# Performance work log

Hardware: AMD Instinct MI355X
Metric: run time of the kernel (lower is better)

The kernel has to match this reference:

```python
import jax, jax.numpy as jnp
import numpy as np

B, NF, EC, H, W = 16, 64, 3, 256, 256
NF1, NF2 = NF // 8, NF // 4  # 8, 16

def _leaky(x):
    return jnp.where(x >= 0, x, 0.2 * x)

def setup_inputs() -> dict:
    key = jax.random.key(0)
    ks = jax.random.split(key, 10)
    s = lambda fan_in: 1.0 / np.sqrt(fan_in)
    return {
        "feature_maps": jax.random.normal(ks[0], (B, NF, H, W), dtype=jnp.float32),
        "extra_maps": jax.random.normal(ks[1], (B, EC, H, W), dtype=jnp.float32),
        "w1": jax.random.uniform(ks[2], (NF1, EC), jnp.float32, -s(EC), s(EC)),
        "b1": jax.random.uniform(ks[3], (NF1,), jnp.float32, -s(EC), s(EC)),
        "w2": jax.random.uniform(ks[4], (NF2, NF1), jnp.float32, -s(NF1), s(NF1)),
        "b2": jax.random.uniform(ks[5], (NF2,), jnp.float32, -s(NF1), s(NF1)),
        "wm": jax.random.uniform(ks[6], (NF, NF2), jnp.float32, -s(NF2), s(NF2)),
        "bm": jax.random.uniform(ks[7], (NF,), jnp.float32, -s(NF2), s(NF2)),
        "wa": jax.random.uniform(ks[8], (NF, NF2), jnp.float32, -s(NF2), s(NF2)),
        "ba": jax.random.uniform(ks[9], (NF,), jnp.float32, -s(NF2), s(NF2)),
    }

def reference(feature_maps, extra_maps, w1, b1, w2, b2, wm, bm, wa, ba):
    # 1x1 convs expressed as channel contractions (per-pixel MLP chain)
    fea1 = _leaky(jnp.einsum('oc,bchw->bohw', w1, extra_maps) + b1[:, None, None])
    fea2 = _leaky(jnp.einsum('oc,bchw->bohw', w2, fea1) + b2[:, None, None])
    mul = jnp.einsum('oc,bchw->bohw', wm, fea2) + bm[:, None, None]
    add = jnp.einsum('oc,bchw->bohw', wa, fea2) + ba[:, None, None]
    # out = add / (1 + feature_maps * mul)
    return add / (1.0 + feature_maps * mul)
```

## Files before the change

kernel.cpp:

```cpp
#include <hip/hip_runtime.h>

#define HW 65536
#define NPIX (16 * HW)
#define THREADS 256


__device__ __forceinline__ double leakyd(double x) {
    return fmax(x, 0.2 * x);
}

__global__ __launch_bounds__(THREADS, 4) void attcnn_kernel(
    const float* __restrict__ fm,
    const float* __restrict__ ex,
    const float* __restrict__ w1,
    const float* __restrict__ b1,
    const float* __restrict__ w2,
    const float* __restrict__ b2,
    const float* __restrict__ wm,
    const float* __restrict__ bm,
    const float* __restrict__ wa,
    const float* __restrict__ ba,
    float* __restrict__ out)
{
    __shared__ double s_w1[24];
    __shared__ double s_b1[8];
    __shared__ double s_w2[128];
    __shared__ double s_b2[16];
    __shared__ double s_wm[1024];
    __shared__ double s_bm[64];
    __shared__ float  s_wa[1024];
    __shared__ float  s_ba[64];

    const int tid = threadIdx.x;
    if (tid < 24)  s_w1[tid] = (double)w1[tid];
    if (tid < 8)   s_b1[tid] = (double)b1[tid];
    if (tid < 128) s_w2[tid] = (double)w2[tid];
    if (tid < 16)  s_b2[tid] = (double)b2[tid];
    if (tid < 64)  { s_bm[tid] = (double)bm[tid]; s_ba[tid] = ba[tid]; }
    #pragma unroll
    for (int i = 0; i < 4; ++i) {
        s_wm[tid + i * 256] = (double)wm[tid + i * 256];
        s_wa[tid + i * 256] = wa[tid + i * 256];
    }
    __syncthreads();

    const int idx = blockIdx.x * THREADS + tid;
    const int b   = idx >> 16;
    const int hw  = idx & 65535;

    const float* exp_ = ex + (long)b * 3 * HW + hw;
    const double e0 = (double)exp_[0];
    const double e1 = (double)exp_[HW];
    const double e2 = (double)exp_[2 * HW];

    double f1v[8];
    #pragma unroll
    for (int j = 0; j < 8; ++j) {
        f1v[j] = leakyd(fma(s_w1[j * 3 + 0], e0,
                        fma(s_w1[j * 3 + 1], e1,
                        fma(s_w1[j * 3 + 2], e2, s_b1[j]))));
    }

    double f2d[16];
    float  f2s[16];
    #pragma unroll
    for (int k = 0; k < 16; ++k) {
        double acc = s_b2[k];
        #pragma unroll
        for (int j = 0; j < 8; ++j)
            acc = fma(s_w2[k * 8 + j], f1v[j], acc);
        acc = leakyd(acc);
        f2d[k] = acc;
        f2s[k] = (float)acc;
    }

    const float* fmp = fm  + (long)b * 64 * HW + hw;
    float*       op  = out + (long)b * 64 * HW + hw;

    float fcur[8], fnxt[8];
    #pragma unroll
    for (int i = 0; i < 8; ++i) fcur[i] = fmp[(long)i * HW];

    #pragma unroll 1
    for (int c = 0; c < 8; ++c) {
        const int ob = c * 8;
        if (c < 7) {
            #pragma unroll
            for (int i = 0; i < 8; ++i)
                fnxt[i] = fmp[(long)(ob + 8 + i) * HW];
        }
        #pragma unroll
        for (int i = 0; i < 8; ++i) {
            const int o = ob + i;
            double m = s_bm[o];
            float  a = s_ba[o];
            #pragma unroll
            for (int k = 0; k < 16; ++k) {
                m = fma(s_wm[o * 16 + k], f2d[k], m);
                a = fmaf(s_wa[o * 16 + k], f2s[k], a);
            }
            const double den = fma((double)fcur[i], m, 1.0);
            float h = (float)den;
            float r = __builtin_amdgcn_rcpf(h);
            r = r * fmaf(-h, r, 2.0f);
            op[(long)o * HW] = a * r;
        }
        if (c < 7) {
            #pragma unroll
            for (int i = 0; i < 8; ++i) fcur[i] = fnxt[i];
        }
    }
}

extern "C" void kernel_launch(void* const* d_in, const int* in_sizes, int n_in,
                              void* d_out, int out_size, void* d_ws, size_t ws_size,
                              hipStream_t stream) {
    const float* fm = (const float*)d_in[0];
    const float* ex = (const float*)d_in[1];
    const float* w1 = (const float*)d_in[2];
    const float* b1 = (const float*)d_in[3];
    const float* w2 = (const float*)d_in[4];
    const float* b2 = (const float*)d_in[5];
    const float* wm = (const float*)d_in[6];
    const float* bm = (const float*)d_in[7];
    const float* wa = (const float*)d_in[8];
    const float* ba = (const float*)d_in[9];
    float* out = (float*)d_out;

    const int blocks = NPIX / THREADS;
    attcnn_kernel<<<blocks, THREADS, 0, stream>>>(fm, ex, w1, b1, w2, b2,
                                                  wm, bm, wa, ba, out);
}
```

Before: 473.3 us.

## Pre-convert weights in a setup kernel, read them uniformly, stream loads nontemporally

Adds a small kernel that converts the weights to double and float once into workspace. The main kernel then reads them straight from global memory with uniform addresses, which the compiler can turn into scalar loads, instead of staging them through shared memory behind a per-block barrier. Feature-map loads and output stores become nontemporal to reduce cache pollution. The mul/add channel dot products are split into two accumulators to shorten FMA dependency chains. This costs one extra kernel launch and relies on scalar caching of the weights.

```diff
diff --git a/kernel.cpp b/kernel.cpp
--- a/kernel.cpp
+++ b/kernel.cpp
@@ -5,46 +5,49 @@
 #define THREADS 256
 
 
+#define DW1 0
+#define DB1 24
+#define DW2 32
+#define DB2 160
+#define DWM 176
+#define DBM 1200
+#define NDBL 1264
+#define FWA 0
+#define FBA 1024
+
 __device__ __forceinline__ double leakyd(double x) {
     return fmax(x, 0.2 * x);
+}
+
+__global__ __launch_bounds__(256) void cvt_weights(
+    const float* __restrict__ w1, const float* __restrict__ b1,
+    const float* __restrict__ w2, const float* __restrict__ b2,
+    const float* __restrict__ wm, const float* __restrict__ bm,
+    const float* __restrict__ wa, const float* __restrict__ ba,
+    double* __restrict__ wd, float* __restrict__ wf)
+{
+    const int t = threadIdx.x;
+    if (t < 24)  wd[DW1 + t] = (double)w1[t];
+    if (t < 8)   wd[DB1 + t] = (double)b1[t];
+    if (t < 128) wd[DW2 + t] = (double)w2[t];
+    if (t < 16)  wd[DB2 + t] = (double)b2[t];
+    if (t < 64)  wd[DBM + t] = (double)bm[t];
+    if (t < 64)  wf[FBA + t] = ba[t];
+    #pragma unroll
+    for (int i = 0; i < 4; ++i) {
+        wd[DWM + t + i * 256] = (double)wm[t + i * 256];
+        wf[FWA + t + i * 256] = wa[t + i * 256];
+    }
 }
 
 __global__ __launch_bounds__(THREADS, 4) void attcnn_kernel(
     const float* __restrict__ fm,
     const float* __restrict__ ex,
-    const float* __restrict__ w1,
-    const float* __restrict__ b1,
-    const float* __restrict__ w2,
-    const float* __restrict__ b2,
-    const float* __restrict__ wm,
-    const float* __restrict__ bm,
-    const float* __restrict__ wa,
-    const float* __restrict__ ba,
+    const double* __restrict__ wd,
+    const float* __restrict__ wf,
     float* __restrict__ out)
 {
-    __shared__ double s_w1[24];
-    __shared__ double s_b1[8];
-    __shared__ double s_w2[128];
-    __shared__ double s_b2[16];
-    __shared__ double s_wm[1024];
-    __shared__ double s_bm[64];
-    __shared__ float  s_wa[1024];
-    __shared__ float  s_ba[64];
-
-    const int tid = threadIdx.x;
-    if (tid < 24)  s_w1[tid] = (double)w1[tid];
-    if (tid < 8)   s_b1[tid] = (double)b1[tid];
-    if (tid < 128) s_w2[tid] = (double)w2[tid];
-    if (tid < 16)  s_b2[tid] = (double)b2[tid];
-    if (tid < 64)  { s_bm[tid] = (double)bm[tid]; s_ba[tid] = ba[tid]; }
-    #pragma unroll
-    for (int i = 0; i < 4; ++i) {
-        s_wm[tid + i * 256] = (double)wm[tid + i * 256];
-        s_wa[tid + i * 256] = wa[tid + i * 256];
-    }
-    __syncthreads();
-
-    const int idx = blockIdx.x * THREADS + tid;
+    const int idx = blockIdx.x * THREADS + threadIdx.x;
     const int b   = idx >> 16;
     const int hw  = idx & 65535;
 
@@ -56,19 +59,19 @@
     double f1v[8];
     #pragma unroll
     for (int j = 0; j < 8; ++j) {
-        f1v[j] = leakyd(fma(s_w1[j * 3 + 0], e0,
-                        fma(s_w1[j * 3 + 1], e1,
-                        fma(s_w1[j * 3 + 2], e2, s_b1[j]))));
+        f1v[j] = leakyd(fma(wd[DW1 + j * 3 + 0], e0,
+                        fma(wd[DW1 + j * 3 + 1], e1,
+                        fma(wd[DW1 + j * 3 + 2], e2, wd[DB1 + j]))));
     }
 
     double f2d[16];
     float  f2s[16];
     #pragma unroll
     for (int k = 0; k < 16; ++k) {
-        double acc = s_b2[k];
+        double acc = wd[DB2 + k];
         #pragma unroll
         for (int j = 0; j < 8; ++j)
-            acc = fma(s_w2[k * 8 + j], f1v[j], acc);
+            acc = fma(wd[DW2 + k * 8 + j], f1v[j], acc);
         acc = leakyd(acc);
         f2d[k] = acc;
         f2s[k] = (float)acc;
@@ -79,7 +82,8 @@
 
     float fcur[8], fnxt[8];
     #pragma unroll
-    for (int i = 0; i < 8; ++i) fcur[i] = fmp[(long)i * HW];
+    for (int i = 0; i < 8; ++i)
+        fcur[i] = __builtin_nontemporal_load(fmp + (long)i * HW);
 
     #pragma unroll 1
     for (int c = 0; c < 8; ++c) {
@@ -87,23 +91,29 @@
         if (c < 7) {
             #pragma unroll
             for (int i = 0; i < 8; ++i)
-                fnxt[i] = fmp[(long)(ob + 8 + i) * HW];
+                fnxt[i] = __builtin_nontemporal_load(fmp + (long)(ob + 8 + i) * HW);
         }
         #pragma unroll
         for (int i = 0; i < 8; ++i) {
             const int o = ob + i;
-            double m = s_bm[o];
-            float  a = s_ba[o];
+            const double* wmr = wd + DWM + o * 16;
+            const float*  war = wf + FWA + o * 16;
+            double m0 = wd[DBM + o], m1 = 0.0;
+            float  a0 = wf[FBA + o], a1 = 0.0f;
             #pragma unroll
-            for (int k = 0; k < 16; ++k) {
-                m = fma(s_wm[o * 16 + k], f2d[k], m);
-                a = fmaf(s_wa[o * 16 + k], f2s[k], a);
+            for (int k = 0; k < 16; k += 2) {
+                m0 = fma(wmr[k],     f2d[k],     m0);
+                m1 = fma(wmr[k + 1], f2d[k + 1], m1);
+                a0 = fmaf(war[k],     f2s[k],     a0);
+                a1 = fmaf(war[k + 1], f2s[k + 1], a1);
             }
+            const double m = m0 + m1;
+            const float  a = a0 + a1;
             const double den = fma((double)fcur[i], m, 1.0);
             float h = (float)den;
             float r = __builtin_amdgcn_rcpf(h);
             r = r * fmaf(-h, r, 2.0f);
-            op[(long)o * HW] = a * r;
+            __builtin_nontemporal_store(a * r, op + (long)o * HW);
         }
         if (c < 7) {
             #pragma unroll
@@ -127,7 +137,11 @@
     const float* ba = (const float*)d_in[9];
     float* out = (float*)d_out;
 
+    double* wd = (double*)d_ws;
+    float*  wf = (float*)(wd + NDBL);
+
+    cvt_weights<<<1, 256, 0, stream>>>(w1, b1, w2, b2, wm, bm, wa, ba, wd, wf);
+
     const int blocks = NPIX / THREADS;
-    attcnn_kernel<<<blocks, THREADS, 0, stream>>>(fm, ex, w1, b1, w2, b2,
-                                                  wm, bm, wa, ba, out);
+    attcnn_kernel<<<blocks, THREADS, 0, stream>>>(fm, ex, wd, wf, out);
 }
```

Measured after the change: 463.4 us. -2.1%, faster.
